# Kernel tuning notes

Hardware: AMD Instinct MI355X
Metric: run time of the kernel (lower is better)

The kernel has to match this reference:

```python
import jax, jax.numpy as jnp
import numpy as np

BN_EPS = 1e-5
NN_EPS = 1e-8
K = 3


def conv_bn_relu(x, W, b, gamma, beta, mean, var):
    # x: [B, Cin, N]; W: [Cout, Cin] (1x1 conv); BN in inference mode w/ running stats
    y = jnp.einsum('bcn,oc->bon', x, W) + b[None, :, None]
    y = (y - mean[None, :, None]) * (gamma / jnp.sqrt(var + BN_EPS))[None, :, None] + beta[None, :, None]
    return jax.nn.relu(y)


def three_interpolation(p1, p2, f2):
    # p1: [B, N1, 3] unknown xyz; p2: [B, N2, 3] known xyz; f2: [B, C, N2]
    # squared pairwise distances via the expansion trick (avoids [B,N1,N2,3])
    d2 = (jnp.sum(p1 * p1, -1)[:, :, None]
          + jnp.sum(p2 * p2, -1)[:, None, :]
          - 2.0 * jnp.einsum('bnd,bmd->bnm', p1, p2))  # [B, N1, N2]
    neg_d2, idx = jax.lax.top_k(-d2, K)                 # 3 nearest
    dist = -neg_d2                                      # squared dists, [B, N1, 3]
    recip = 1.0 / (dist + NN_EPS)
    weight = recip / jnp.sum(recip, axis=-1, keepdims=True)  # [B, N1, 3]
    f2t = jnp.transpose(f2, (0, 2, 1))                  # [B, N2, C]
    gathered = jax.vmap(lambda f, i: f[i])(f2t, idx)    # [B, N1, 3, C]
    return jnp.einsum('bnkc,bnk->bcn', gathered, weight)  # [B, C, N1]


def setup_inputs() -> dict:
    key = jax.random.key(0)
    ks = jax.random.split(key, 16)
    B, N1, N2 = 8, 16384, 4096
    mlp = [256, 128, 128]
    inp = {
        'p1': jax.random.normal(ks[0], (B, N1, 3), jnp.float32),
        'p2': jax.random.normal(ks[1], (B, N2, 3), jnp.float32),
        'f2': jax.random.normal(ks[2], (B, mlp[0], N2), jnp.float32),
    }
    kidx = 3
    for li in range(len(mlp) - 1):
        cin, cout = mlp[li], mlp[li + 1]
        inp[f'W{li}'] = jax.random.normal(ks[kidx], (cout, cin), jnp.float32) * (1.0 / np.sqrt(cin)); kidx += 1
        inp[f'b{li}'] = jnp.zeros((cout,), jnp.float32)
        inp[f'gamma{li}'] = jnp.ones((cout,), jnp.float32)
        inp[f'beta{li}'] = jnp.zeros((cout,), jnp.float32)
        inp[f'mean{li}'] = jax.random.normal(ks[kidx], (cout,), jnp.float32) * 0.1; kidx += 1
        inp[f'var{li}'] = jax.random.uniform(ks[kidx], (cout,), jnp.float32, 0.5, 1.5); kidx += 1
    return inp


def reference(p1, p2, f2,
              W0, b0, gamma0, beta0, mean0, var0,
              W1, b1, gamma1, beta1, mean1, var1):
    f = conv_bn_relu(f2, W0, b0, gamma0, beta0, mean0, var0)
    f = conv_bn_relu(f, W1, b1, gamma1, beta1, mean1, var1)
    return three_interpolation(p1, p2, f)
```

## Files before the change

### kernel.cpp

```cpp
#include <hip/hip_runtime.h>

#define B_    8
#define N1_   16384
#define N2_   4096
#define NTOT_ (B_ * N1_)

__device__ __forceinline__ float np_sumsq(float x, float y, float z)
{
#pragma clang fp contract(off)
    return ((x * x + y * y) + z * z);
}

__global__ __launch_bounds__(256) void prep_kernel(
    const float* __restrict__ W0, const float* __restrict__ b0,
    const float* __restrict__ g0, const float* __restrict__ be0,
    const float* __restrict__ m0, const float* __restrict__ v0,
    const float* __restrict__ W1, const float* __restrict__ b1,
    const float* __restrict__ g1, const float* __restrict__ be1,
    const float* __restrict__ m1, const float* __restrict__ v1,
    const float* __restrict__ p2,
    float* __restrict__ W0p, float* __restrict__ b0p,
    float* __restrict__ W1p, float* __restrict__ b1p,
    float4* __restrict__ q4)
{
    const int bx = blockIdx.x;
    const int tid = threadIdx.x;
    if (bx < 128) {
        const int t = bx * 256 + tid;
        const int o = t >> 8;
        const float s = g0[o] / sqrtf(v0[o] + 1e-5f);
        W0p[t] = W0[t] * s;
        if (t < 128) {
            const float ss = g0[t] / sqrtf(v0[t] + 1e-5f);
            b0p[t] = be0[t] + (b0[t] - m0[t]) * ss;
        }
    } else if (bx < 192) {
        const int t = (bx - 128) * 256 + tid;
        const int o = t >> 7;
        const float s = g1[o] / sqrtf(v1[o] + 1e-5f);
        W1p[t] = W1[t] * s;
        if (t < 128) {
            const float ss = g1[t] / sqrtf(v1[t] + 1e-5f);
            b1p[t] = be1[t] + (b1[t] - m1[t]) * ss;
        }
    } else {
        const int t = (bx - 192) * 256 + tid;
        const float x = p2[3 * (size_t)t + 0];
        const float y = p2[3 * (size_t)t + 1];
        const float z = p2[3 * (size_t)t + 2];
        q4[t] = make_float4(x, y, z, np_sumsq(x, y, z));
    }
}

template <int CIN, bool TRANS>
__global__ __launch_bounds__(256) void gemm_relu_kernel(
    const float* __restrict__ X, const float* __restrict__ Wp,
    const float* __restrict__ bp, float* __restrict__ Y)
{
    __shared__ float A_lds[32][136];
    __shared__ float B_lds[32][64];

    const int b  = blockIdx.y;
    const int n0 = blockIdx.x * 64;
    const int tid = threadIdx.x;
    const int ty = tid >> 4;
    const int tx = tid & 15;
    const float* Xb = X + (size_t)b * CIN * N2_;

    float acc[8][4];
#pragma unroll
    for (int i = 0; i < 8; ++i)
#pragma unroll
        for (int j = 0; j < 4; ++j) acc[i][j] = 0.f;

    const int a_kq = (tid & 7) * 4;
    const int a_r0 = tid >> 3;
    const int b_n4 = (tid & 15) * 4;
    const int b_k0 = tid >> 4;

    for (int k0 = 0; k0 < CIN; k0 += 32) {
#pragma unroll
        for (int i = 0; i < 4; ++i) {
            const int row = a_r0 + 32 * i;
            const float4 v = *(const float4*)&Wp[(size_t)row * CIN + k0 + a_kq];
            A_lds[a_kq + 0][row] = v.x;
            A_lds[a_kq + 1][row] = v.y;
            A_lds[a_kq + 2][row] = v.z;
            A_lds[a_kq + 3][row] = v.w;
        }
#pragma unroll
        for (int i = 0; i < 2; ++i) {
            const int krow = b_k0 + 16 * i;
            *(float4*)&B_lds[krow][b_n4] =
                *(const float4*)&Xb[(size_t)(k0 + krow) * N2_ + n0 + b_n4];
        }
        __syncthreads();

#pragma unroll
        for (int kk = 0; kk < 32; ++kk) {
            const float4 a0 = *(const float4*)&A_lds[kk][ty * 4];
            const float4 a1 = *(const float4*)&A_lds[kk][64 + ty * 4];
            const float4 bq = *(const float4*)&B_lds[kk][tx * 4];
            const float av[8] = {a0.x, a0.y, a0.z, a0.w, a1.x, a1.y, a1.z, a1.w};
            const float bv[4] = {bq.x, bq.y, bq.z, bq.w};
#pragma unroll
            for (int i = 0; i < 8; ++i)
#pragma unroll
                for (int j = 0; j < 4; ++j)
                    acc[i][j] = fmaf(av[i], bv[j], acc[i][j]);
        }
        __syncthreads();
    }

    float bias_v[8];
#pragma unroll
    for (int i = 0; i < 8; ++i) {
        const int r = (i < 4) ? (ty * 4 + i) : (64 + ty * 4 + (i - 4));
        bias_v[i] = bp[r];
    }

    if (!TRANS) {
#pragma unroll
        for (int i = 0; i < 8; ++i) {
            const int r = (i < 4) ? (ty * 4 + i) : (64 + ty * 4 + (i - 4));
            float* yrow = Y + ((size_t)b * 128 + r) * N2_ + n0;
            float4 v0;
            v0.x = fmaxf(acc[i][0] + bias_v[i], 0.f);
            v0.y = fmaxf(acc[i][1] + bias_v[i], 0.f);
            v0.z = fmaxf(acc[i][2] + bias_v[i], 0.f);
            v0.w = fmaxf(acc[i][3] + bias_v[i], 0.f);
            *(float4*)(yrow + tx * 4) = v0;
        }
    } else {
        float (*T)[132] = (float(*)[132])&A_lds[0][0];
#pragma unroll
        for (int s = 0; s < 2; ++s) {
            if ((tx >> 3) == s) {
                const int cl0 = (tx & 7) * 4;
#pragma unroll
                for (int i = 0; i < 8; ++i) {
                    const int r = (i < 4) ? (ty * 4 + i) : (64 + ty * 4 + (i - 4));
#pragma unroll
                    for (int j = 0; j < 4; ++j)
                        T[cl0 + j][r] = fmaxf(acc[i][j] + bias_v[i], 0.f);
                }
            }
            __syncthreads();
#pragma unroll
            for (int p = 0; p < 4; ++p) {
                const int row = (tid >> 5) + 8 * p;
                const float4 v = *(const float4*)&T[row][(tid & 31) * 4];
                float* orow = Y + ((size_t)b * N2_ + n0 + 32 * s + row) * 128;
                *(float4*)&orow[(tid & 31) * 4] = v;
            }
            __syncthreads();
        }
    }
}

__global__ __launch_bounds__(256, 8) void knn_phase1(
    const float* __restrict__ p1, const float4* __restrict__ q4,
    float* __restrict__ part_d, int* __restrict__ part_i)
{
    __shared__ float4 qs[1024];
    const int tid = threadIdx.x;
    const int chunk = blockIdx.x & 3;
    const int g = (blockIdx.x >> 2) * 256 + tid;
    const int b = g >> 14;

    const float px = p1[3 * (size_t)g + 0];
    const float py = p1[3 * (size_t)g + 1];
    const float pz = p1[3 * (size_t)g + 2];
    const float s1 = np_sumsq(px, py, pz);

    const float4* qb = q4 + (size_t)b * N2_ + chunk * 1024;
#pragma unroll
    for (int i = 0; i < 4; ++i) qs[tid + i * 256] = qb[tid + i * 256];
    __syncthreads();

    float d0 = 1e30f, d1 = 1e30f, d2v = 1e30f;
    int i0 = 0, i1 = 0, i2 = 0;
    const int jbase = chunk * 1024;

    for (int j = 0; j < 1024; j += 4) {
#pragma unroll
        for (int u = 0; u < 4; ++u) {
            const float4 q = qs[j + u];
            const float dot = __fmaf_rn(px, q.x, __fmaf_rn(py, q.y, __fmul_rn(pz, q.z)));
            const float ss  = s1 + q.w;
            const float t   = __fmaf_rn(-2.0f, dot, ss);
            if (t < d2v) {
                const int jj = jbase + j + u;
                const bool c1 = t < d1, c0 = t < d0;
                d2v = c1 ? d1 : t;                 i2 = c1 ? i1 : jj;
                const float nd1 = c1 ? (c0 ? d0 : t) : d1;
                const int   ni1 = c1 ? (c0 ? i0 : jj) : i1;
                d1 = nd1;                          i1 = ni1;
                d0 = c0 ? t : d0;                  i0 = c0 ? jj : i0;
            }
        }
    }

    part_d[(0 * 4 + chunk) * NTOT_ + g] = d0;
    part_d[(1 * 4 + chunk) * NTOT_ + g] = d1;
    part_d[(2 * 4 + chunk) * NTOT_ + g] = d2v;
    part_i[(0 * 4 + chunk) * NTOT_ + g] = i0;
    part_i[(1 * 4 + chunk) * NTOT_ + g] = i1;
    part_i[(2 * 4 + chunk) * NTOT_ + g] = i2;
}

__global__ __launch_bounds__(256) void gather_kernel(
    const float* __restrict__ f_t, const float* __restrict__ part_d,
    const int* __restrict__ part_i, float* __restrict__ out)
{
    __shared__ float T[64][129];
    const int tid = threadIdx.x;
    const int lane = tid & 63, wv = tid >> 6;
    const int vb = (blockIdx.x & 7) * 256 + (blockIdx.x >> 3);
    const int gbase = vb * 64;
    const int g = gbase + lane;
    const int b = g >> 14, n0 = gbase & 16383;

    float d0 = 1e30f, d1 = 1e30f, d2v = 1e30f;
    int i0 = 0, i1 = 0, i2 = 0;
#pragma unroll
    for (int c = 0; c < 4; ++c) {
#pragma unroll
        for (int k = 0; k < 3; ++k) {
            const float t = part_d[(k * 4 + c) * NTOT_ + g];
            const int  jj = part_i[(k * 4 + c) * NTOT_ + g];
            if (t < d2v) {
                const bool c1 = t < d1, c0 = t < d0;
                d2v = c1 ? d1 : t;                 i2 = c1 ? i1 : jj;
                const float nd1 = c1 ? (c0 ? d0 : t) : d1;
                const int   ni1 = c1 ? (c0 ? i0 : jj) : i1;
                d1 = nd1;                          i1 = ni1;
                d0 = c0 ? t : d0;                  i0 = c0 ? jj : i0;
            }
        }
    }

    float w0, w1, w2;
    {
#pragma clang fp contract(off)
        const float r0 = 1.0f / (d0 + 1e-8f);
        const float r1 = 1.0f / (d1 + 1e-8f);
        const float r2 = 1.0f / (d2v + 1e-8f);
        const float rs = (r0 + r1) + r2;
        w0 = r0 / rs;
        w1 = r1 / rs;
        w2 = r2 / rs;
    }

    const float* fb = f_t + (size_t)b * N2_ * 128;
#pragma unroll
    for (int j = 0; j < 16; ++j) {
        const int q = wv * 16 + j;
        const int   qi0 = __shfl(i0, q);
        const int   qi1 = __shfl(i1, q);
        const int   qi2 = __shfl(i2, q);
        const float qw0 = __shfl(w0, q);
        const float qw1 = __shfl(w1, q);
        const float qw2 = __shfl(w2, q);
        const float2 a  = *(const float2*)(fb + (size_t)qi0 * 128 + 2 * lane);
        const float2 bb = *(const float2*)(fb + (size_t)qi1 * 128 + 2 * lane);
        const float2 c  = *(const float2*)(fb + (size_t)qi2 * 128 + 2 * lane);
        T[q][2 * lane + 0] = fmaf(qw0, a.x, fmaf(qw1, bb.x, qw2 * c.x));
        T[q][2 * lane + 1] = fmaf(qw0, a.y, fmaf(qw1, bb.y, qw2 * c.y));
    }
    __syncthreads();

    float* ob = out + ((size_t)b * 128) * N1_ + n0 + lane;
#pragma unroll
    for (int ci = 0; ci < 32; ++ci) {
        const int cch = wv * 32 + ci;
        __builtin_nontemporal_store(T[lane][cch], ob + (size_t)cch * N1_);
    }
}

extern "C" void kernel_launch(void* const* d_in, const int* in_sizes, int n_in,
                              void* d_out, int out_size, void* d_ws, size_t ws_size,
                              hipStream_t stream)
{
    const float* p1  = (const float*)d_in[0];
    const float* p2  = (const float*)d_in[1];
    const float* f2  = (const float*)d_in[2];
    const float* W0  = (const float*)d_in[3];
    const float* b0  = (const float*)d_in[4];
    const float* g0  = (const float*)d_in[5];
    const float* be0 = (const float*)d_in[6];
    const float* m0  = (const float*)d_in[7];
    const float* v0  = (const float*)d_in[8];
    const float* W1  = (const float*)d_in[9];
    const float* b1  = (const float*)d_in[10];
    const float* g1  = (const float*)d_in[11];
    const float* be1 = (const float*)d_in[12];
    const float* m1  = (const float*)d_in[13];
    const float* v1  = (const float*)d_in[14];

    char* ws = (char*)d_ws;
    float4* q4  = (float4*)(ws);
    float*  W0p = (float*)(ws + (512 << 10));
    float*  b0p = (float*)(ws + (640 << 10));
    float*  W1p = (float*)(ws + (644 << 10));
    float*  b1p = (float*)(ws + (708 << 10));
    float*  h   = (float*)(ws + ((size_t)1 << 20));
    float*  f_t = (float*)(ws + ((size_t)17 << 20));
    float*  pd  = (float*)(ws + ((size_t)1 << 20));
    int*    pi  = (int*)  (ws + ((size_t)9 << 20));

    prep_kernel<<<320, 256, 0, stream>>>(W0, b0, g0, be0, m0, v0,
                                         W1, b1, g1, be1, m1, v1,
                                         p2, W0p, b0p, W1p, b1p, q4);

    gemm_relu_kernel<256, false><<<dim3(64, 8), 256, 0, stream>>>(f2, W0p, b0p, h);
    gemm_relu_kernel<128, true ><<<dim3(64, 8), 256, 0, stream>>>(h, W1p, b1p, f_t);

    knn_phase1<<<(NTOT_ / 256) * 4, 256, 0, stream>>>(p1, q4, pd, pi);
    gather_kernel<<<NTOT_ / 64, 256, 0, stream>>>(f_t, pd, pi, (float*)d_out);
}
```

Before: 333.3 us.

## Fuse the two 1x1 conv GEMMs into one kernel keeping hidden activations in LDS

Merges the two conv+BN+ReLU GEMM kernels into a single kernel. Each block computes a 128-column tile of the first layer, writes the ReLU output into a large LDS tile, and runs the second GEMM directly from LDS. This removes the global round trip of the intermediate h tensor and one launch. Per-thread register tiles grow from 8x4 to 8x8. The grid shrinks to 256 blocks and LDS use rises to about 85KB per block, so occupancy and parallelism drop.

```diff
diff --git a/kernel.cpp b/kernel.cpp
--- a/kernel.cpp
+++ b/kernel.cpp
@@ -52,97 +52,148 @@
     }
 }
 
-template <int CIN, bool TRANS>
-__global__ __launch_bounds__(256) void gemm_relu_kernel(
-    const float* __restrict__ X, const float* __restrict__ Wp,
-    const float* __restrict__ bp, float* __restrict__ Y)
+__global__ __launch_bounds__(256) void gemm_fused_kernel(
+    const float* __restrict__ f2, const float* __restrict__ W0p,
+    const float* __restrict__ b0p, const float* __restrict__ W1p,
+    const float* __restrict__ b1p, float* __restrict__ f_t)
 {
     __shared__ float A_lds[32][136];
-    __shared__ float B_lds[32][64];
+    __shared__ float HT[128][132];
+    float (*B_lds)[128] = (float(*)[128])&HT[0][0];
 
     const int b  = blockIdx.y;
-    const int n0 = blockIdx.x * 64;
+    const int n0 = blockIdx.x * 128;
     const int tid = threadIdx.x;
     const int ty = tid >> 4;
     const int tx = tid & 15;
-    const float* Xb = X + (size_t)b * CIN * N2_;
-
-    float acc[8][4];
-#pragma unroll
-    for (int i = 0; i < 8; ++i)
-#pragma unroll
-        for (int j = 0; j < 4; ++j) acc[i][j] = 0.f;
+
+    float acc[8][8];
 
     const int a_kq = (tid & 7) * 4;
     const int a_r0 = tid >> 3;
-    const int b_n4 = (tid & 15) * 4;
-    const int b_k0 = tid >> 4;
-
-    for (int k0 = 0; k0 < CIN; k0 += 32) {
+    const int b_n4 = (tid & 31) * 4;
+    const int b_k0 = tid >> 5;
+
+#pragma unroll
+    for (int i = 0; i < 8; ++i)
+#pragma unroll
+        for (int j = 0; j < 8; ++j) acc[i][j] = 0.f;
+
+    {
+        const float* Xb = f2 + (size_t)b * 256 * N2_;
+        for (int k0 = 0; k0 < 256; k0 += 32) {
+#pragma unroll
+            for (int i = 0; i < 4; ++i) {
+                const int row = a_r0 + 32 * i;
+                const float4 v = *(const float4*)&W0p[(size_t)row * 256 + k0 + a_kq];
+                A_lds[a_kq + 0][row] = v.x;
+                A_lds[a_kq + 1][row] = v.y;
+                A_lds[a_kq + 2][row] = v.z;
+                A_lds[a_kq + 3][row] = v.w;
+            }
+#pragma unroll
+            for (int i = 0; i < 4; ++i) {
+                const int krow = b_k0 + 8 * i;
+                *(float4*)&B_lds[krow][b_n4] =
+                    *(const float4*)&Xb[(size_t)(k0 + krow) * N2_ + n0 + b_n4];
+            }
+            __syncthreads();
+
+#pragma unroll
+            for (int kk = 0; kk < 32; ++kk) {
+                const float4 a0 = *(const float4*)&A_lds[kk][ty * 4];
+                const float4 a1 = *(const float4*)&A_lds[kk][64 + ty * 4];
+                const float4 bq0 = *(const float4*)&B_lds[kk][tx * 4];
+                const float4 bq1 = *(const float4*)&B_lds[kk][64 + tx * 4];
+                const float av[8] = {a0.x, a0.y, a0.z, a0.w, a1.x, a1.y, a1.z, a1.w};
+                const float bv[8] = {bq0.x, bq0.y, bq0.z, bq0.w, bq1.x, bq1.y, bq1.z, bq1.w};
+#pragma unroll
+                for (int i = 0; i < 8; ++i)
+#pragma unroll
+                    for (int j = 0; j < 8; ++j)
+                        acc[i][j] = fmaf(av[i], bv[j], acc[i][j]);
+            }
+            __syncthreads();
+        }
+    }
+
+    {
+        float bias_v[8];
+#pragma unroll
+        for (int i = 0; i < 8; ++i) {
+            const int r = (i < 4) ? (ty * 4 + i) : (64 + ty * 4 + (i - 4));
+            bias_v[i] = b0p[r];
+        }
+#pragma unroll
+        for (int i = 0; i < 8; ++i) {
+            const int r = (i < 4) ? (ty * 4 + i) : (64 + ty * 4 + (i - 4));
+            float4 v0, v1;
+            v0.x = fmaxf(acc[i][0] + bias_v[i], 0.f);
+            v0.y = fmaxf(acc[i][1] + bias_v[i], 0.f);
+            v0.z = fmaxf(acc[i][2] + bias_v[i], 0.f);
+            v0.w = fmaxf(acc[i][3] + bias_v[i], 0.f);
+            v1.x = fmaxf(acc[i][4] + bias_v[i], 0.f);
+            v1.y = fmaxf(acc[i][5] + bias_v[i], 0.f);
+            v1.z = fmaxf(acc[i][6] + bias_v[i], 0.f);
+            v1.w = fmaxf(acc[i][7] + bias_v[i], 0.f);
+            *(float4*)&HT[r][tx * 4] = v0;
+            *(float4*)&HT[r][64 + tx * 4] = v1;
+        }
+    }
+
+#pragma unroll
+    for (int i = 0; i < 8; ++i)
+#pragma unroll
+        for (int j = 0; j < 8; ++j) acc[i][j] = 0.f;
+
+    for (int k0 = 0; k0 < 128; k0 += 32) {
 #pragma unroll
         for (int i = 0; i < 4; ++i) {
             const int row = a_r0 + 32 * i;
-            const float4 v = *(const float4*)&Wp[(size_t)row * CIN + k0 + a_kq];
+            const float4 v = *(const float4*)&W1p[(size_t)row * 128 + k0 + a_kq];
             A_lds[a_kq + 0][row] = v.x;
             A_lds[a_kq + 1][row] = v.y;
             A_lds[a_kq + 2][row] = v.z;
             A_lds[a_kq + 3][row] = v.w;
         }
-#pragma unroll
-        for (int i = 0; i < 2; ++i) {
-            const int krow = b_k0 + 16 * i;
-            *(float4*)&B_lds[krow][b_n4] =
-                *(const float4*)&Xb[(size_t)(k0 + krow) * N2_ + n0 + b_n4];
-        }
         __syncthreads();
 
 #pragma unroll
         for (int kk = 0; kk < 32; ++kk) {
             const float4 a0 = *(const float4*)&A_lds[kk][ty * 4];
             const float4 a1 = *(const float4*)&A_lds[kk][64 + ty * 4];
-            const float4 bq = *(const float4*)&B_lds[kk][tx * 4];
+            const float4 bq0 = *(const float4*)&HT[k0 + kk][tx * 4];
+            const float4 bq1 = *(const float4*)&HT[k0 + kk][64 + tx * 4];
             const float av[8] = {a0.x, a0.y, a0.z, a0.w, a1.x, a1.y, a1.z, a1.w};
-            const float bv[4] = {bq.x, bq.y, bq.z, bq.w};
+            const float bv[8] = {bq0.x, bq0.y, bq0.z, bq0.w, bq1.x, bq1.y, bq1.z, bq1.w};
 #pragma unroll
             for (int i = 0; i < 8; ++i)
 #pragma unroll
-                for (int j = 0; j < 4; ++j)
+                for (int j = 0; j < 8; ++j)
                     acc[i][j] = fmaf(av[i], bv[j], acc[i][j]);
         }
         __syncthreads();
     }
 
-    float bias_v[8];
-#pragma unroll
-    for (int i = 0; i < 8; ++i) {
-        const int r = (i < 4) ? (ty * 4 + i) : (64 + ty * 4 + (i - 4));
-        bias_v[i] = bp[r];
-    }
-
-    if (!TRANS) {
+    {
+        float bias_v[8];
 #pragma unroll
         for (int i = 0; i < 8; ++i) {
             const int r = (i < 4) ? (ty * 4 + i) : (64 + ty * 4 + (i - 4));
-            float* yrow = Y + ((size_t)b * 128 + r) * N2_ + n0;
-            float4 v0;
-            v0.x = fmaxf(acc[i][0] + bias_v[i], 0.f);
-            v0.y = fmaxf(acc[i][1] + bias_v[i], 0.f);
-            v0.z = fmaxf(acc[i][2] + bias_v[i], 0.f);
-            v0.w = fmaxf(acc[i][3] + bias_v[i], 0.f);
-            *(float4*)(yrow + tx * 4) = v0;
-        }
-    } else {
+            bias_v[i] = b1p[r];
+        }
         float (*T)[132] = (float(*)[132])&A_lds[0][0];
 #pragma unroll
-        for (int s = 0; s < 2; ++s) {
-            if ((tx >> 3) == s) {
+        for (int s = 0; s < 4; ++s) {
+            if ((tx >> 3) == (s & 1)) {
+                const int joff = (s >> 1) * 4;
                 const int cl0 = (tx & 7) * 4;
 #pragma unroll
                 for (int i = 0; i < 8; ++i) {
                     const int r = (i < 4) ? (ty * 4 + i) : (64 + ty * 4 + (i - 4));
 #pragma unroll
                     for (int j = 0; j < 4; ++j)
-                        T[cl0 + j][r] = fmaxf(acc[i][j] + bias_v[i], 0.f);
+                        T[cl0 + j][r] = fmaxf(acc[i][j + joff] + bias_v[i], 0.f);
                 }
             }
             __syncthreads();
@@ -150,7 +201,7 @@
             for (int p = 0; p < 4; ++p) {
                 const int row = (tid >> 5) + 8 * p;
                 const float4 v = *(const float4*)&T[row][(tid & 31) * 4];
-                float* orow = Y + ((size_t)b * N2_ + n0 + 32 * s + row) * 128;
+                float* orow = f_t + ((size_t)b * N2_ + n0 + 32 * s + row) * 128;
                 *(float4*)&orow[(tid & 31) * 4] = v;
             }
             __syncthreads();
@@ -304,7 +355,6 @@
     float*  b0p = (float*)(ws + (640 << 10));
     float*  W1p = (float*)(ws + (644 << 10));
     float*  b1p = (float*)(ws + (708 << 10));
-    float*  h   = (float*)(ws + ((size_t)1 << 20));
     float*  f_t = (float*)(ws + ((size_t)17 << 20));
     float*  pd  = (float*)(ws + ((size_t)1 << 20));
     int*    pi  = (int*)  (ws + ((size_t)9 << 20));
@@ -313,8 +363,8 @@
                                          W1, b1, g1, be1, m1, v1,
                                          p2, W0p, b0p, W1p, b1p, q4);
 
-    gemm_relu_kernel<256, false><<<dim3(64, 8), 256, 0, stream>>>(f2, W0p, b0p, h);
-    gemm_relu_kernel<128, true ><<<dim3(64, 8), 256, 0, stream>>>(h, W1p, b1p, f_t);
+    gemm_fused_kernel<<<dim3(32, 8), 256, 0, stream>>>(f2, W0p, b0p,
+                                                       W1p, b1p, f_t);
 
     knn_phase1<<<(NTOT_ / 256) * 4, 256, 0, stream>>>(p1, q4, pd, pi);
     gather_kernel<<<NTOT_ / 64, 256, 0, stream>>>(f_t, pd, pi, (float*)d_out);
```

New measurement: 325.2 us. -2.5%, faster.
